# Kernel optimization log

Hardware: AMD Instinct MI355X
Metric: run time of the kernel (lower is better)

## Reference

```python
import jax, jax.numpy as jnp
import numpy as np

N = 100_000  # nodes
E = 1_200_000  # edges (avg degree 12)
EPS = 1e-5


def setup_inputs() -> dict:
    key = jax.random.key(0)
    ks = jax.random.split(key, 12)

    def w(k, shape):
        fan_in = shape[0]
        return jax.random.normal(k, shape, dtype=jnp.float32) * (1.0 / np.sqrt(fan_in))

    return {
        "x": jax.random.normal(ks[0], (N, 4), dtype=jnp.float32),
        "edge_index": jax.random.randint(ks[1], (2, E), 0, N, dtype=jnp.int32),
        "W1": w(ks[2], (4, 16)), "b1": jnp.zeros(16, jnp.float32),
        "g1": jnp.ones(16, jnp.float32), "bt1": jnp.zeros(16, jnp.float32),
        "W2": w(ks[3], (16, 32)), "b2": jnp.zeros(32, jnp.float32),
        "g2": jnp.ones(32, jnp.float32), "bt2": jnp.zeros(32, jnp.float32),
        "W3": w(ks[4], (32, 64)), "b3": jnp.zeros(64, jnp.float32),
        "g3": jnp.ones(64, jnp.float32), "bt3": jnp.zeros(64, jnp.float32),
        "Wf1": w(ks[5], (64, 32)), "bf1": jnp.zeros(32, jnp.float32),
        "Wf2": w(ks[6], (32, 16)), "bf2": jnp.zeros(16, jnp.float32),
        "Wf3": w(ks[7], (16, 2)), "bf3": jnp.zeros(2, jnp.float32),
    }


def _gcn_conv(x, W, b, src, dst):
    """PyG GCNConv: self-loops + symmetric deg^-1/2 normalization + scatter-add."""
    n = x.shape[0]
    h = x @ W  # [N, out]
    loop = jnp.arange(n, dtype=src.dtype)
    s = jnp.concatenate([src, loop])  # [E+N]
    d = jnp.concatenate([dst, loop])
    deg = jax.ops.segment_sum(jnp.ones_like(d, dtype=h.dtype), d, num_segments=n)
    dinv = jnp.where(deg > 0, jax.lax.rsqrt(deg), 0.0)
    norm = dinv[s] * dinv[d]  # [E+N]
    out = jax.ops.segment_sum(h[s] * norm[:, None], d, num_segments=n)
    return out + b


def _bn(x, g, bt):
    # BatchNorm1d over node dim (batch statistics, training-mode semantics)
    m = jnp.mean(x, axis=0)
    v = jnp.var(x, axis=0)
    return (x - m) * jax.lax.rsqrt(v + EPS) * g + bt


def reference(x, edge_index, W1, b1, g1, bt1, W2, b2, g2, bt2, W3, b3, g3, bt3,
              Wf1, bf1, Wf2, bf2, Wf3, bf3):
    src, dst = edge_index[0], edge_index[1]
    h = jax.nn.elu(_bn(jax.nn.relu(_gcn_conv(x, W1, b1, src, dst)), g1, bt1))
    h = jax.nn.elu(_bn(jax.nn.relu(_gcn_conv(h, W2, b2, src, dst)), g2, bt2))
    h = jax.nn.elu(_bn(jax.nn.relu(_gcn_conv(h, W3, b3, src, dst)), g3, bt3))
    h = jax.nn.elu(h @ Wf1 + bf1)
    h = jax.nn.elu(h @ Wf2 + bf2)
    h = h @ Wf3 + bf3
    return jax.nn.log_softmax(h, axis=1)
```

## Files before the change

### kernel.cpp

```cpp
#include <hip/hip_runtime.h>
#include <hip/hip_fp16.h>
#include <math.h>

#define BN_EPS 1e-5f

union H8 {
  float4 f4;
  __half2 h2[4];
};


#define NHB 512

__global__ void hist_kernel(const int* __restrict__ dst, int* __restrict__ histpart, int e) {
  __shared__ int h[512];
  for (int i = threadIdx.x; i < 512; i += 256) h[i] = 0;
  __syncthreads();
  int stride = gridDim.x * 256;
  for (int i = blockIdx.x * 256 + threadIdx.x; i < e; i += stride)
    atomicAdd(&h[dst[i] >> 8], 1);
  __syncthreads();
  for (int i = threadIdx.x; i < 512; i += 256)
    histpart[blockIdx.x * 512 + i] = h[i];
}

__global__ void scan_buckets(const int* __restrict__ histpart,
                             int* __restrict__ boffset, int* __restrict__ bcursor,
                             int* __restrict__ row_start, int nbuck, int n, int e) {
  __shared__ int sc[512];
  int tid = threadIdx.x;
  int v = 0;
  for (int r = 0; r < NHB; r++) v += histpart[r * 512 + tid];
  sc[tid] = v;
  __syncthreads();
  for (int off = 1; off < 512; off <<= 1) {
    int add = (tid >= off) ? sc[tid - off] : 0;
    __syncthreads();
    sc[tid] += add;
    __syncthreads();
  }
  int excl = sc[tid] - v;
  if (tid <= nbuck) {
    int val = (tid < nbuck) ? excl : e;
    boffset[tid] = val;
    bcursor[tid] = val;
  }
  if (tid == 0) row_start[n] = e;
}

__global__ void partition_kernel(const int* __restrict__ src, const int* __restrict__ dst,
                                 int* __restrict__ bcursor, int* __restrict__ ebuf, int e) {
  __shared__ int h[512];
  __shared__ int base[512];
  const int BLK_E = 4096;
  int e0 = blockIdx.x * BLK_E;
  int e1 = min(e0 + BLK_E, e);
  for (int i = threadIdx.x; i < 512; i += 256) h[i] = 0;
  __syncthreads();
  for (int i = e0 + threadIdx.x; i < e1; i += 256)
    atomicAdd(&h[dst[i] >> 8], 1);
  __syncthreads();
  for (int i = threadIdx.x; i < 512; i += 256) {
    int c = h[i];
    base[i] = (c > 0) ? atomicAdd(&bcursor[i], c) : 0;
    h[i] = 0;
  }
  __syncthreads();
  for (int i = e0 + threadIdx.x; i < e1; i += 256) {
    int d = dst[i];
    int b = d >> 8;
    int r = atomicAdd(&h[b], 1);
    ebuf[base[b] + r] = (src[i] << 8) | (d & 255);
  }
}

__global__ void bucket_fill(const int* __restrict__ ebuf, const int* __restrict__ boffset,
                            int* __restrict__ row_start, float* __restrict__ dinv,
                            int* __restrict__ csr_src, int n) {
  __shared__ int lcnt[256];
  __shared__ int lpre[256];
  int bid = blockIdx.x;
  int nb0 = bid << 8;
  int tid = threadIdx.x;
  int e0 = boffset[bid], e1 = boffset[bid + 1];
  lcnt[tid] = 0;
  __syncthreads();
  for (int j = e0 + tid; j < e1; j += 256)
    atomicAdd(&lcnt[ebuf[j] & 255], 1);
  __syncthreads();
  int v = lcnt[tid];
  lpre[tid] = v;
  __syncthreads();
  for (int off = 1; off < 256; off <<= 1) {
    int add = (tid >= off) ? lpre[tid - off] : 0;
    __syncthreads();
    lpre[tid] += add;
    __syncthreads();
  }
  int excl = lpre[tid] - v;
  int node = nb0 + tid;
  if (node < n) {
    row_start[node] = e0 + excl;
    dinv[node] = rsqrtf((float)(v + 1));
  }
  __syncthreads();
  lpre[tid] = excl;
  __syncthreads();
  for (int j = e0 + tid; j < e1; j += 256) {
    int ed = ebuf[j];
    int p = atomicAdd(&lpre[ed & 255], 1);
    csr_src[e0 + p] = ed >> 8;
  }
}

template <int K, int C, bool BN>
__global__ __launch_bounds__(256) void mm_dinv_h(
    const float* __restrict__ X, const float* __restrict__ stats,
    const float* __restrict__ g, const float* __restrict__ bt,
    const float* __restrict__ W, const float* __restrict__ dinv,
    float4* __restrict__ hh, int n) {
  constexpr int GP8 = C / 8;
  __shared__ float w[K * C];
  __shared__ float bsc[K], bsh[K];
  for (int i = threadIdx.x; i < K * C; i += 256) w[i] = W[i];
  if (BN && threadIdx.x < K) {
    int c = threadIdx.x;
    float inv_n = 1.0f / (float)n;
    float m = stats[c] * inv_n;
    float var = fmaxf(stats[K + c] * inv_n - m * m, 0.f);
    float sc = rsqrtf(var + BN_EPS) * g[c];
    bsc[c] = sc;
    bsh[c] = bt[c] - m * sc;
  }
  __syncthreads();

  int idx = blockIdx.x * 256 + threadIdx.x;
  if (idx >= n * GP8) return;
  int nn = idx / GP8;
  int c8 = idx % GP8;

  float acc[8];
#pragma unroll
  for (int t = 0; t < 8; t++) acc[t] = 0.f;

  const float4* row4 = (const float4*)(X + (size_t)nn * K);
#pragma unroll
  for (int k4 = 0; k4 < K / 4; k4++) {
    float4 xv = row4[k4];
#pragma unroll
    for (int j = 0; j < 4; j++) {
      int k = k4 * 4 + j;
      float v = (j == 0) ? xv.x : (j == 1) ? xv.y : (j == 2) ? xv.z : xv.w;
      if (BN) {
        v = v * bsc[k] + bsh[k];
        v = v > 0.f ? v : (expf(v) - 1.f);
      }
      int wb = k * C + c8 * 8;
#pragma unroll
      for (int t = 0; t < 8; t++) acc[t] += v * w[wb + t];
    }
  }
  float dn = dinv[nn];
  H8 o;
#pragma unroll
  for (int q = 0; q < 4; q++)
    o.h2[q] = __float22half2_rn(make_float2(acc[2 * q] * dn, acc[2 * q + 1] * dn));
  hh[idx] = o.f4;
}

template <int C, int LOGGP>
__global__ __launch_bounds__(256) void gather_finalize_h(
    const float4* __restrict__ hh8, const int* __restrict__ row_start,
    const int* __restrict__ csr_src, const float* __restrict__ dinv,
    const float* __restrict__ bias, float4* __restrict__ act4,
    float* __restrict__ partials, int n) {
  constexpr int GP = C / 8;
  constexpr int GP4 = C / 4;
  constexpr int NPB = 256 / GP;
  int tid = threadIdx.x;
  int c8 = tid & (GP - 1);
  int local = tid >> LOGGP;
  int n0 = blockIdx.x * NPB + local;
  bool valid = (n0 < n);

  float vo[8];
#pragma unroll
  for (int t = 0; t < 8; t++) vo[t] = 0.f;

  if (valid) {
    float acc[8];
    {
      H8 u;
      u.f4 = hh8[n0 * GP + c8];
#pragma unroll
      for (int q = 0; q < 4; q++) {
        float2 f = __half22float2(u.h2[q]);
        acc[2 * q] = f.x;
        acc[2 * q + 1] = f.y;
      }
    }
    int s = row_start[n0], e0 = row_start[n0 + 1];
    int j = s;
    for (; j + 8 <= e0; j += 8) {
      H8 u[8];
#pragma unroll
      for (int m = 0; m < 8; m++) u[m].f4 = hh8[csr_src[j + m] * GP + c8];
#pragma unroll
      for (int m = 0; m < 8; m++)
#pragma unroll
        for (int q = 0; q < 4; q++) {
          float2 f = __half22float2(u[m].h2[q]);
          acc[2 * q] += f.x;
          acc[2 * q + 1] += f.y;
        }
    }
    for (; j + 4 <= e0; j += 4) {
      H8 u[4];
#pragma unroll
      for (int m = 0; m < 4; m++) u[m].f4 = hh8[csr_src[j + m] * GP + c8];
#pragma unroll
      for (int m = 0; m < 4; m++)
#pragma unroll
        for (int q = 0; q < 4; q++) {
          float2 f = __half22float2(u[m].h2[q]);
          acc[2 * q] += f.x;
          acc[2 * q + 1] += f.y;
        }
    }
    for (; j < e0; j++) {
      H8 u;
      u.f4 = hh8[csr_src[j] * GP + c8];
#pragma unroll
      for (int q = 0; q < 4; q++) {
        float2 f = __half22float2(u.h2[q]);
        acc[2 * q] += f.x;
        acc[2 * q + 1] += f.y;
      }
    }

    float dn = dinv[n0];
    const float4* bias4 = (const float4*)bias;
    float4 blo = bias4[c8 * 2], bhi = bias4[c8 * 2 + 1];
    vo[0] = fmaxf(dn * acc[0] + blo.x, 0.f);
    vo[1] = fmaxf(dn * acc[1] + blo.y, 0.f);
    vo[2] = fmaxf(dn * acc[2] + blo.z, 0.f);
    vo[3] = fmaxf(dn * acc[3] + blo.w, 0.f);
    vo[4] = fmaxf(dn * acc[4] + bhi.x, 0.f);
    vo[5] = fmaxf(dn * acc[5] + bhi.y, 0.f);
    vo[6] = fmaxf(dn * acc[6] + bhi.z, 0.f);
    vo[7] = fmaxf(dn * acc[7] + bhi.w, 0.f);
    act4[n0 * GP4 + c8 * 2] = make_float4(vo[0], vo[1], vo[2], vo[3]);
    act4[n0 * GP4 + c8 * 2 + 1] = make_float4(vo[4], vo[5], vo[6], vo[7]);
  }

  __shared__ float redS[8 * 256];
  __shared__ float redQ[8 * 256];
#pragma unroll
  for (int t = 0; t < 8; t++) {
    redS[t * 256 + tid] = vo[t];
    redQ[t * 256 + tid] = vo[t] * vo[t];
  }
#pragma unroll
  for (int off = NPB / 2; off >= 1; off >>= 1) {
    __syncthreads();
    if (local < off) {
#pragma unroll
      for (int t = 0; t < 8; t++) {
        redS[t * 256 + tid] += redS[t * 256 + tid + off * GP];
        redQ[t * 256 + tid] += redQ[t * 256 + tid + off * GP];
      }
    }
  }
  __syncthreads();
  if (local == 0) {
#pragma unroll
    for (int t = 0; t < 8; t++) {
      partials[(size_t)blockIdx.x * 2 * C + c8 * 8 + t] = redS[t * 256 + tid];
      partials[(size_t)blockIdx.x * 2 * C + C + c8 * 8 + t] = redQ[t * 256 + tid];
    }
  }
}

template <int C2>
__global__ void reduce_partials(const float* __restrict__ partials,
                                float* __restrict__ stats, int rows) {
  int ch = blockIdx.x;
  float acc = 0.f;
  for (int r = threadIdx.x; r < rows; r += 256)
    acc += partials[(size_t)r * C2 + ch];
  __shared__ float red[256];
  red[threadIdx.x] = acc;
  __syncthreads();
#pragma unroll
  for (int off = 128; off >= 1; off >>= 1) {
    if (threadIdx.x < off) red[threadIdx.x] += red[threadIdx.x + off];
    __syncthreads();
  }
  if (threadIdx.x == 0) stats[ch] = red[0];
}


__global__ __launch_bounds__(256) void head_kernel(
    const float* __restrict__ h,
    const float* __restrict__ st3, const float* __restrict__ g3,
    const float* __restrict__ bt3,
    const float* __restrict__ Wf1, const float* __restrict__ bf1,
    const float* __restrict__ Wf2, const float* __restrict__ bf2,
    const float* __restrict__ Wf3, const float* __restrict__ bf3,
    float* __restrict__ out, int n) {
  __shared__ float w1[64 * 32], w2[32 * 16], w3[16 * 2];
  __shared__ float sb1[32], sb2[16], sb3[2];
  __shared__ float bsc[64], bsh[64];
  for (int i = threadIdx.x; i < 64 * 32; i += 256) w1[i] = Wf1[i];
  for (int i = threadIdx.x; i < 32 * 16; i += 256) w2[i] = Wf2[i];
  if (threadIdx.x < 64) {
    int c = threadIdx.x;
    float inv_n = 1.0f / (float)n;
    float m = st3[c] * inv_n;
    float var = fmaxf(st3[64 + c] * inv_n - m * m, 0.f);
    float sc = rsqrtf(var + BN_EPS) * g3[c];
    bsc[c] = sc;
    bsh[c] = bt3[c] - m * sc;
  }
  if (threadIdx.x < 32) {
    w3[threadIdx.x] = Wf3[threadIdx.x];
    sb1[threadIdx.x] = bf1[threadIdx.x];
  }
  if (threadIdx.x < 16) sb2[threadIdx.x] = bf2[threadIdx.x];
  if (threadIdx.x < 2) sb3[threadIdx.x] = bf3[threadIdx.x];
  __syncthreads();

  int n0 = blockIdx.x * 256 + threadIdx.x;
  if (n0 >= n) return;

  const float4* h4 = (const float4*)(h + (size_t)n0 * 64);

  float a1[32];
#pragma unroll
  for (int c = 0; c < 32; c++) a1[c] = sb1[c];

#pragma unroll
  for (int k4 = 0; k4 < 16; k4++) {
    float4 hv = h4[k4];
#pragma unroll
    for (int j = 0; j < 4; j++) {
      int k = k4 * 4 + j;
      float hk = (j == 0) ? hv.x : (j == 1) ? hv.y : (j == 2) ? hv.z : hv.w;
      float v = hk * bsc[k] + bsh[k];
      v = v > 0.f ? v : (expf(v) - 1.f);
#pragma unroll
      for (int c = 0; c < 32; c++) a1[c] += v * w1[k * 32 + c];
    }
  }
#pragma unroll
  for (int c = 0; c < 32; c++) {
    float v = a1[c];
    a1[c] = v > 0.f ? v : (expf(v) - 1.f);
  }

  float a2[16];
#pragma unroll
  for (int c = 0; c < 16; c++) {
    float acc = sb2[c];
#pragma unroll
    for (int k = 0; k < 32; k++) acc += a1[k] * w2[k * 16 + c];
    a2[c] = acc > 0.f ? acc : (expf(acc) - 1.f);
  }
  float z0 = sb3[0], z1 = sb3[1];
#pragma unroll
  for (int k = 0; k < 16; k++) {
    z0 += a2[k] * w3[k * 2 + 0];
    z1 += a2[k] * w3[k * 2 + 1];
  }
  float mx = fmaxf(z0, z1);
  float lse = mx + logf(expf(z0 - mx) + expf(z1 - mx));
  out[n0 * 2 + 0] = z0 - lse;
  out[n0 * 2 + 1] = z1 - lse;
}


extern "C" void kernel_launch(void* const* d_in, const int* in_sizes, int n_in,
                              void* d_out, int out_size, void* d_ws, size_t ws_size,
                              hipStream_t stream) {
  const float* x = (const float*)d_in[0];
  const int* ei = (const int*)d_in[1];
  const float* W1 = (const float*)d_in[2];  const float* b1 = (const float*)d_in[3];
  const float* g1 = (const float*)d_in[4];  const float* bt1 = (const float*)d_in[5];
  const float* W2 = (const float*)d_in[6];  const float* b2 = (const float*)d_in[7];
  const float* g2 = (const float*)d_in[8];  const float* bt2 = (const float*)d_in[9];
  const float* W3 = (const float*)d_in[10]; const float* b3 = (const float*)d_in[11];
  const float* g3 = (const float*)d_in[12]; const float* bt3 = (const float*)d_in[13];
  const float* Wf1 = (const float*)d_in[14]; const float* bf1 = (const float*)d_in[15];
  const float* Wf2 = (const float*)d_in[16]; const float* bf2 = (const float*)d_in[17];
  const float* Wf3 = (const float*)d_in[18]; const float* bf3 = (const float*)d_in[19];
  float* out = (float*)d_out;

  const int N = in_sizes[0] / 4;
  const int E = in_sizes[1] / 2;
  const int* srcp = ei;
  const int* dstp = ei + E;
  const int NBUCK = (N + 255) >> 8;

  char* ws = (char*)d_ws;
  size_t off = 0;
  auto alloc = [&](size_t bytes) {
    off = (off + 255) & ~(size_t)255;
    size_t o = off;
    off += bytes;
    return o;
  };
  float* dinv      = (float*)(ws + alloc((size_t)N * 4));
  int*   row_start = (int*)  (ws + alloc((size_t)(N + 1) * 4));
  int*   histpart  = (int*)  (ws + alloc((size_t)NHB * 512 * 4));
  float* stats     = (float*)(ws + alloc((size_t)224 * 4));
  int*   boffset   = (int*)  (ws + alloc((size_t)513 * 4));
  int*   bcursor   = (int*)  (ws + alloc((size_t)513 * 4));
  int*   csr_src   = (int*)  (ws + alloc((size_t)E * 4));
  float* partials  = (float*)(ws + alloc((size_t)3200 * 128 * 4));
  float* bufH      = (float*)(ws + alloc((size_t)N * 64 * 2));
  float* bufAct    = (float*)(ws + alloc((size_t)N * 64 * 4));
  float* st1 = stats;
  float* st2 = stats + 32;
  float* st3 = stats + 96;
  int*   ebuf = (int*)bufH;

  int nb256 = (N + 255) / 256;

  hist_kernel<<<NHB, 256, 0, stream>>>(dstp, histpart, E);
  scan_buckets<<<1, 512, 0, stream>>>(histpart, boffset, bcursor, row_start, NBUCK, N, E);
  partition_kernel<<<(E + 4095) / 4096, 256, 0, stream>>>(srcp, dstp, bcursor, ebuf, E);
  bucket_fill<<<NBUCK, 256, 0, stream>>>(ebuf, boffset, row_start, dinv, csr_src, N);

  int g1n = (N + 127) / 128;
  mm_dinv_h<4, 16, false><<<(N * 2 + 255) / 256, 256, 0, stream>>>(
      x, nullptr, nullptr, nullptr, W1, dinv, (float4*)bufH, N);
  gather_finalize_h<16, 1><<<g1n, 256, 0, stream>>>(
      (const float4*)bufH, row_start, csr_src, dinv, b1, (float4*)bufAct, partials, N);
  reduce_partials<32><<<32, 256, 0, stream>>>(partials, st1, g1n);

  int g2n = (N + 63) / 64;
  mm_dinv_h<16, 32, true><<<(N * 4 + 255) / 256, 256, 0, stream>>>(
      bufAct, st1, g1, bt1, W2, dinv, (float4*)bufH, N);
  gather_finalize_h<32, 2><<<g2n, 256, 0, stream>>>(
      (const float4*)bufH, row_start, csr_src, dinv, b2, (float4*)bufAct, partials, N);
  reduce_partials<64><<<64, 256, 0, stream>>>(partials, st2, g2n);

  int g3n = (N + 31) / 32;
  mm_dinv_h<32, 64, true><<<(N * 8 + 255) / 256, 256, 0, stream>>>(
      bufAct, st2, g2, bt2, W3, dinv, (float4*)bufH, N);
  gather_finalize_h<64, 3><<<g3n, 256, 0, stream>>>(
      (const float4*)bufH, row_start, csr_src, dinv, b3, (float4*)bufAct, partials, N);
  reduce_partials<128><<<128, 256, 0, stream>>>(partials, st3, g3n);

  head_kernel<<<nb256, 256, 0, stream>>>(bufAct, st3, g3, bt3,
                                         Wf1, bf1, Wf2, bf2, Wf3, bf3, out, N);
}
```

Before: 216.0 us.

## Store layer-3 activations as fp16 and split head MLP across two threads per node

```diff
diff --git a/kernel.cpp b/kernel.cpp
--- a/kernel.cpp
+++ b/kernel.cpp
@@ -153,7 +153,7 @@
       float v = (j == 0) ? xv.x : (j == 1) ? xv.y : (j == 2) ? xv.z : xv.w;
       if (BN) {
         v = v * bsc[k] + bsh[k];
-        v = v > 0.f ? v : (expf(v) - 1.f);
+        v = v > 0.f ? v : (__expf(v) - 1.f);
       }
       int wb = k * C + c8 * 8;
 #pragma unroll
@@ -168,7 +168,7 @@
   hh[idx] = o.f4;
 }
 
-template <int C, int LOGGP>
+template <int C, int LOGGP, bool OUTH>
 __global__ __launch_bounds__(256) void gather_finalize_h(
     const float4* __restrict__ hh8, const int* __restrict__ row_start,
     const int* __restrict__ csr_src, const float* __restrict__ dinv,
@@ -249,8 +249,16 @@
     vo[5] = fmaxf(dn * acc[5] + bhi.y, 0.f);
     vo[6] = fmaxf(dn * acc[6] + bhi.z, 0.f);
     vo[7] = fmaxf(dn * acc[7] + bhi.w, 0.f);
-    act4[n0 * GP4 + c8 * 2] = make_float4(vo[0], vo[1], vo[2], vo[3]);
-    act4[n0 * GP4 + c8 * 2 + 1] = make_float4(vo[4], vo[5], vo[6], vo[7]);
+    if (OUTH) {
+      H8 o;
+#pragma unroll
+      for (int q = 0; q < 4; q++)
+        o.h2[q] = __float22half2_rn(make_float2(vo[2 * q], vo[2 * q + 1]));
+      act4[(size_t)n0 * GP + c8] = o.f4;
+    } else {
+      act4[n0 * GP4 + c8 * 2] = make_float4(vo[0], vo[1], vo[2], vo[3]);
+      act4[n0 * GP4 + c8 * 2 + 1] = make_float4(vo[4], vo[5], vo[6], vo[7]);
+    }
   }
 
   __shared__ float redS[8 * 256];
@@ -301,81 +309,101 @@
 
 
 __global__ __launch_bounds__(256) void head_kernel(
-    const float* __restrict__ h,
+    const float4* __restrict__ h16,
     const float* __restrict__ st3, const float* __restrict__ g3,
     const float* __restrict__ bt3,
     const float* __restrict__ Wf1, const float* __restrict__ bf1,
     const float* __restrict__ Wf2, const float* __restrict__ bf2,
     const float* __restrict__ Wf3, const float* __restrict__ bf3,
     float* __restrict__ out, int n) {
-  __shared__ float w1[64 * 32], w2[32 * 16], w3[16 * 2];
+  __shared__ float w1[64 * 32], w2[32 * 16], w3[32];
   __shared__ float sb1[32], sb2[16], sb3[2];
   __shared__ float bsc[64], bsh[64];
-  for (int i = threadIdx.x; i < 64 * 32; i += 256) w1[i] = Wf1[i];
-  for (int i = threadIdx.x; i < 32 * 16; i += 256) w2[i] = Wf2[i];
-  if (threadIdx.x < 64) {
-    int c = threadIdx.x;
+  __shared__ float a1s[32][128];
+  __shared__ float a2s[16][128];
+  int tid = threadIdx.x;
+  for (int i = tid; i < 64 * 32; i += 256) w1[i] = Wf1[i];
+  for (int i = tid; i < 32 * 16; i += 256) w2[i] = Wf2[i];
+  if (tid < 64) {
     float inv_n = 1.0f / (float)n;
-    float m = st3[c] * inv_n;
-    float var = fmaxf(st3[64 + c] * inv_n - m * m, 0.f);
-    float sc = rsqrtf(var + BN_EPS) * g3[c];
-    bsc[c] = sc;
-    bsh[c] = bt3[c] - m * sc;
-  }
-  if (threadIdx.x < 32) {
-    w3[threadIdx.x] = Wf3[threadIdx.x];
-    sb1[threadIdx.x] = bf1[threadIdx.x];
-  }
-  if (threadIdx.x < 16) sb2[threadIdx.x] = bf2[threadIdx.x];
-  if (threadIdx.x < 2) sb3[threadIdx.x] = bf3[threadIdx.x];
-  __syncthreads();
-
-  int n0 = blockIdx.x * 256 + threadIdx.x;
-  if (n0 >= n) return;
-
-  const float4* h4 = (const float4*)(h + (size_t)n0 * 64);
-
-  float a1[32];
-#pragma unroll
-  for (int c = 0; c < 32; c++) a1[c] = sb1[c];
-
-#pragma unroll
-  for (int k4 = 0; k4 < 16; k4++) {
-    float4 hv = h4[k4];
-#pragma unroll
-    for (int j = 0; j < 4; j++) {
-      int k = k4 * 4 + j;
-      float hk = (j == 0) ? hv.x : (j == 1) ? hv.y : (j == 2) ? hv.z : hv.w;
-      float v = hk * bsc[k] + bsh[k];
-      v = v > 0.f ? v : (expf(v) - 1.f);
-#pragma unroll
-      for (int c = 0; c < 32; c++) a1[c] += v * w1[k * 32 + c];
-    }
-  }
-#pragma unroll
-  for (int c = 0; c < 32; c++) {
+    float m = st3[tid] * inv_n;
+    float var = fmaxf(st3[64 + tid] * inv_n - m * m, 0.f);
+    float sc = rsqrtf(var + BN_EPS) * g3[tid];
+    bsc[tid] = sc;
+    bsh[tid] = bt3[tid] - m * sc;
+  }
+  if (tid < 32) {
+    w3[tid] = Wf3[tid];
+    sb1[tid] = bf1[tid];
+  }
+  if (tid < 16) sb2[tid] = bf2[tid];
+  if (tid < 2) sb3[tid] = bf3[tid];
+  __syncthreads();
+
+  int node = tid & 127;
+  int half = tid >> 7;
+  int n0 = blockIdx.x * 128 + node;
+  bool valid = (n0 < n);
+
+  float a1[16];
+#pragma unroll
+  for (int c = 0; c < 16; c++) a1[c] = sb1[half * 16 + c];
+  if (valid) {
+    const float4* hrow = h16 + (size_t)n0 * 8;
+#pragma unroll
+    for (int j = 0; j < 8; j++) {
+      H8 u;
+      u.f4 = hrow[j];
+#pragma unroll
+      for (int q = 0; q < 4; q++) {
+        float2 f = __half22float2(u.h2[q]);
+        int k0 = j * 8 + 2 * q, k1 = k0 + 1;
+        float v0 = f.x * bsc[k0] + bsh[k0];
+        v0 = v0 > 0.f ? v0 : (__expf(v0) - 1.f);
+        float v1 = f.y * bsc[k1] + bsh[k1];
+        v1 = v1 > 0.f ? v1 : (__expf(v1) - 1.f);
+#pragma unroll
+        for (int c = 0; c < 16; c++)
+          a1[c] += v0 * w1[k0 * 32 + half * 16 + c] + v1 * w1[k1 * 32 + half * 16 + c];
+      }
+    }
+  }
+#pragma unroll
+  for (int c = 0; c < 16; c++) {
     float v = a1[c];
-    a1[c] = v > 0.f ? v : (expf(v) - 1.f);
-  }
-
-  float a2[16];
-#pragma unroll
-  for (int c = 0; c < 16; c++) {
-    float acc = sb2[c];
-#pragma unroll
-    for (int k = 0; k < 32; k++) acc += a1[k] * w2[k * 16 + c];
-    a2[c] = acc > 0.f ? acc : (expf(acc) - 1.f);
-  }
-  float z0 = sb3[0], z1 = sb3[1];
-#pragma unroll
-  for (int k = 0; k < 16; k++) {
-    z0 += a2[k] * w3[k * 2 + 0];
-    z1 += a2[k] * w3[k * 2 + 1];
-  }
-  float mx = fmaxf(z0, z1);
-  float lse = mx + logf(expf(z0 - mx) + expf(z1 - mx));
-  out[n0 * 2 + 0] = z0 - lse;
-  out[n0 * 2 + 1] = z1 - lse;
+    a1s[half * 16 + c][node] = v > 0.f ? v : (__expf(v) - 1.f);
+  }
+  __syncthreads();
+
+  float a2[8];
+#pragma unroll
+  for (int c = 0; c < 8; c++) a2[c] = sb2[half * 8 + c];
+#pragma unroll
+  for (int k = 0; k < 32; k++) {
+    float ak = a1s[k][node];
+#pragma unroll
+    for (int c = 0; c < 8; c++) a2[c] += ak * w2[k * 16 + half * 8 + c];
+  }
+#pragma unroll
+  for (int c = 0; c < 8; c++) {
+    float v = a2[c];
+    a2s[half * 8 + c][node] = v > 0.f ? v : (__expf(v) - 1.f);
+  }
+  __syncthreads();
+
+  if (half == 0 && valid) {
+    float z0 = sb3[0], z1 = sb3[1];
+#pragma unroll
+    for (int k = 0; k < 16; k++) {
+      float ak = a2s[k][node];
+      z0 += ak * w3[k * 2 + 0];
+      z1 += ak * w3[k * 2 + 1];
+    }
+    float mx = fmaxf(z0, z1);
+    float lse = mx + __logf(__expf(z0 - mx) + __expf(z1 - mx));
+    out[(size_t)n0 * 2 + 0] = z0 - lse;
+    out[(size_t)n0 * 2 + 1] = z1 - lse;
+  }
 }
 
 
@@ -424,8 +452,6 @@
   float* st3 = stats + 96;
   int*   ebuf = (int*)bufH;
 
-  int nb256 = (N + 255) / 256;
-
   hist_kernel<<<NHB, 256, 0, stream>>>(dstp, histpart, E);
   scan_buckets<<<1, 512, 0, stream>>>(histpart, boffset, bcursor, row_start, NBUCK, N, E);
   partition_kernel<<<(E + 4095) / 4096, 256, 0, stream>>>(srcp, dstp, bcursor, ebuf, E);
@@ -434,24 +460,24 @@
   int g1n = (N + 127) / 128;
   mm_dinv_h<4, 16, false><<<(N * 2 + 255) / 256, 256, 0, stream>>>(
       x, nullptr, nullptr, nullptr, W1, dinv, (float4*)bufH, N);
-  gather_finalize_h<16, 1><<<g1n, 256, 0, stream>>>(
+  gather_finalize_h<16, 1, false><<<g1n, 256, 0, stream>>>(
       (const float4*)bufH, row_start, csr_src, dinv, b1, (float4*)bufAct, partials, N);
   reduce_partials<32><<<32, 256, 0, stream>>>(partials, st1, g1n);
 
   int g2n = (N + 63) / 64;
   mm_dinv_h<16, 32, true><<<(N * 4 + 255) / 256, 256, 0, stream>>>(
       bufAct, st1, g1, bt1, W2, dinv, (float4*)bufH, N);
-  gather_finalize_h<32, 2><<<g2n, 256, 0, stream>>>(
+  gather_finalize_h<32, 2, false><<<g2n, 256, 0, stream>>>(
       (const float4*)bufH, row_start, csr_src, dinv, b2, (float4*)bufAct, partials, N);
   reduce_partials<64><<<64, 256, 0, stream>>>(partials, st2, g2n);
 
   int g3n = (N + 31) / 32;
   mm_dinv_h<32, 64, true><<<(N * 8 + 255) / 256, 256, 0, stream>>>(
       bufAct, st2, g2, bt2, W3, dinv, (float4*)bufH, N);
-  gather_finalize_h<64, 3><<<g3n, 256, 0, stream>>>(
+  gather_finalize_h<64, 3, true><<<g3n, 256, 0, stream>>>(
       (const float4*)bufH, row_start, csr_src, dinv, b3, (float4*)bufAct, partials, N);
   reduce_partials<128><<<128, 256, 0, stream>>>(partials, st3, g3n);
 
-  head_kernel<<<nb256, 256, 0, stream>>>(bufAct, st3, g3, bt3,
-                                         Wf1, bf1, Wf2, bf2, Wf3, bf3, out, N);
-}
+  head_kernel<<<(N + 127) / 128, 256, 0, stream>>>(
+      (const float4*)bufAct, st3, g3, bt3, Wf1, bf1, Wf2, bf2, Wf3, bf3, out, N);
+}
```

After: 198.4 us. 8.2% less time.
